# Kernel tuning notes

Hardware: AMD Instinct MI355X
Metric: run time of the kernel (lower is better)

Reference implementation:

```python
import jax, jax.numpy as jnp
from jax import lax
import numpy as np

EPS = 1e-5


def _fps(xyz, S):
    B, N, _ = xyz.shape

    def step(carry, _):
        dist, far = carry  # [B,N], [B]
        c = xyz[jnp.arange(B), far]               # [B,3]
        d = jnp.sum((xyz - c[:, None, :]) ** 2, -1)  # [B,N]
        dist = jnp.minimum(dist, d)
        nxt = jnp.argmax(dist, -1).astype(jnp.int32)
        return (dist, nxt), far

    init = (jnp.full((B, N), 1e10, xyz.dtype), jnp.zeros((B,), jnp.int32))
    _, idxs = lax.scan(step, init, None, length=S)
    return jnp.transpose(idxs)  # [B,S]


def _gather(pts, idx):
    # pts: [B,N,C], idx: [B,...] -> [B,...,C]
    return jax.vmap(lambda p, i: p[i])(pts, idx)


def _conv(x, W, b):
    # 1x1 Conv1d: x [M,Cin,L], W [Cout,Cin], b [Cout]
    return jnp.einsum('mcl,oc->mol', x, W) + b[None, :, None]


def _bn(x, g, b):
    # BatchNorm1d (training-mode batch stats, biased variance)
    mu = jnp.mean(x, (0, 2), keepdims=True)
    v = jnp.var(x, (0, 2), keepdims=True)
    return g[None, :, None] * (x - mu) / jnp.sqrt(v + EPS) + b[None, :, None]


def _forward(xyz, feature, affine_alpha, affine_beta, w_tr, b_tr, g_tr, be_tr,
             w1, b1, g1, be1, w2, b2, groups, k):
    xyz = jnp.transpose(xyz, (0, 2, 1))        # [B,N,3]
    feature = jnp.transpose(feature, (0, 2, 1))  # [B,N,D]
    B, N, _ = xyz.shape
    S = groups
    xyz_ng = lax.stop_gradient(xyz)  # cluster() runs under torch.no_grad
    fps_idx = _fps(xyz_ng, S)                        # [B,S]
    new_xyz = _gather(xyz_ng, fps_idx)               # [B,S,3] (detached)
    # squared-distance kNN: [B,S,N]
    sqr = (jnp.sum(new_xyz ** 2, -1)[:, :, None]
           + jnp.sum(xyz_ng ** 2, -1)[:, None, :]
           - 2.0 * jnp.einsum('bsc,bnc->bsn', new_xyz, xyz_ng))
    _, idx = lax.top_k(-sqr, k)                      # [B,S,k] smallest distances
    new_feature = _gather(feature, fps_idx)          # [B,S,D]
    grouped_xyz = _gather(xyz, idx)                  # [B,S,k,3]
    grouped_feature = _gather(feature, idx)          # [B,S,k,D]
    grouped_feature = jnp.concatenate([grouped_feature, grouped_xyz], -1)  # [B,S,k,D+3]
    # anchor normalization
    mean = jnp.concatenate([new_feature, new_xyz], -1)[:, :, None, :]  # [B,S,1,D+3]
    diff = grouped_feature - mean
    std = jnp.std(diff.reshape(B, -1), axis=-1, ddof=1)[:, None, None, None]
    gf = affine_alpha * (diff / (std + EPS)) + affine_beta
    # concat anchor feature -> [B,S,k,2D+3]
    D = new_feature.shape[-1]
    x = jnp.concatenate([gf, jnp.broadcast_to(new_feature[:, :, None, :], (B, S, k, D))], -1)
    d = x.shape[-1]
    # PreExtraction: [B,S,k,d] -> [B*S,d,k]
    x = jnp.transpose(x, (0, 1, 3, 2)).reshape(B * S, d, k)
    x = jax.nn.relu(_bn(_conv(x, w_tr, b_tr), g_tr, be_tr))
    y = jax.nn.relu(_bn(_conv(x, w1, b1), g1, be1))
    y = _conv(y, w2, b2)
    x = jax.nn.relu(y + x)
    x = jnp.max(x, -1).reshape(B, S, -1)             # adaptive_max_pool1d(1)
    return (jnp.transpose(new_xyz, (0, 2, 1)), jnp.transpose(x, (0, 2, 1)))


def setup_inputs() -> dict:
    key = jax.random.key(0)
    k0, k1, k2, k3, k4 = jax.random.split(key, 5)
    B, N, D = 8, 4096, 64
    return {
        'xyz': jax.random.normal(k0, (B, 3, N), jnp.float32),
        'feature': jax.random.normal(k1, (B, D, N), jnp.float32),
        'affine_alpha': jnp.ones((1, 1, 1, D + 3), jnp.float32),
        'affine_beta': jnp.zeros((1, 1, 1, D + 3), jnp.float32),
        'w_tr': 0.05 * jax.random.normal(k2, (D, 3 + 2 * D), jnp.float32),
        'b_tr': jnp.zeros((D,), jnp.float32),
        'g_tr': jnp.ones((D,), jnp.float32),
        'be_tr': jnp.zeros((D,), jnp.float32),
        'w1': 0.05 * jax.random.normal(k3, (D, D), jnp.float32),
        'b1': jnp.zeros((D,), jnp.float32),
        'g1': jnp.ones((D,), jnp.float32),
        'be1': jnp.zeros((D,), jnp.float32),
        'w2': 0.05 * jax.random.normal(k4, (D, D), jnp.float32),
        'b2': jnp.zeros((D,), jnp.float32),
        'groups': 1024,
        'k': 32,
    }


def reference(xyz, feature, affine_alpha, affine_beta, w_tr, b_tr, g_tr, be_tr,
              w1, b1, g1, be1, w2, b2, groups, k):
    return _forward(xyz, feature, affine_alpha, affine_beta, w_tr, b_tr, g_tr, be_tr,
                    w1, b1, g1, be1, w2, b2, groups, k)
```

## Files before the change

### kernel.cpp

```cpp
#include <hip/hip_runtime.h>
#include <cfloat>
#include <math.h>

#define B_ 8
#define N_ 4096
#define D_ 64
#define S_ 1024
#define K_ 32
#define CIN_ 131

template <int CTRL>
__device__ __forceinline__ unsigned long long dpp_u64(unsigned long long k) {
  int lo = (int)(unsigned int)k, hi = (int)(unsigned int)(k >> 32);
  lo = __builtin_amdgcn_update_dpp(lo, lo, CTRL, 0xf, 0xf, false);
  hi = __builtin_amdgcn_update_dpp(hi, hi, CTRL, 0xf, 0xf, false);
  return ((unsigned long long)(unsigned int)hi << 32) | (unsigned int)lo;
}

__device__ __forceinline__ float wave_max_f32_dpp(float v) {
  int x = __float_as_int(v);
#define STEP(ctrl)                                                        \
  {                                                                       \
    int t = __builtin_amdgcn_update_dpp(x, x, ctrl, 0xf, 0xf, false);     \
    v = fmaxf(v, __int_as_float(t));                                      \
    x = __float_as_int(v);                                                \
  }
  STEP(0x111)
  STEP(0x112)
  STEP(0x114)
  STEP(0x118)
  STEP(0x142)
  STEP(0x143)
#undef STEP
  return __int_as_float(__builtin_amdgcn_readlane(x, 63));
}

__global__ __launch_bounds__(256) void fps_kernel(const float* __restrict__ xyz,
                                                  int* __restrict__ fps_idx,
                                                  float* __restrict__ nxyz,
                                                  float* __restrict__ out0,
                                                  const float* __restrict__ feature,
                                                  float* __restrict__ featT) {
  const int tid = threadIdx.x;
  __shared__ __align__(16) float4 sp[N_];
  __shared__ int si[S_];
  __shared__ unsigned long long keyp[2][4];
  if (blockIdx.x >= 8) {
    const int blk = blockIdx.x - 8;
    const int b = blk >> 6, n0 = (blk & 63) * 64;
    float* tile = (float*)sp;
#pragma unroll
    for (int i = 0; i < 16; i++) {
      int c = i * 4 + (tid >> 6), nl = tid & 63;
      tile[c * 65 + nl] = feature[((size_t)b * 64 + c) * N_ + n0 + nl];
    }
    __syncthreads();
#pragma unroll
    for (int i = 0; i < 16; i++) {
      int nl = i * 4 + (tid >> 6), c = tid & 63;
      featT[((size_t)b * N_ + n0 + nl) * 64 + c] = tile[c * 65 + nl];
    }
    return;
  }
  const int b = blockIdx.x;
  const float* xb = xyz + (size_t)b * 3 * N_;
  const float4* xv = (const float4*)xb;
  float px[16], py[16], pz[16], dist[16];
#pragma unroll
  for (int q = 0; q < 4; q++) {
    float4 X = xv[4 * tid + q];
    float4 Y = xv[1024 + 4 * tid + q];
    float4 Z = xv[2048 + 4 * tid + q];
    px[4 * q + 0] = X.x; px[4 * q + 1] = X.y; px[4 * q + 2] = X.z; px[4 * q + 3] = X.w;
    py[4 * q + 0] = Y.x; py[4 * q + 1] = Y.y; py[4 * q + 2] = Y.z; py[4 * q + 3] = Y.w;
    pz[4 * q + 0] = Z.x; pz[4 * q + 1] = Z.y; pz[4 * q + 2] = Z.z; pz[4 * q + 3] = Z.w;
  }
#pragma unroll
  for (int i = 0; i < 16; i++) {
    dist[i] = 1e10f;
    sp[16 * tid + i] = make_float4(px[i], py[i], pz[i], 0.f);
  }
  if (tid == 0) si[0] = 0;
  __syncthreads();
  float cx = sp[0].x, cy = sp[0].y, cz = sp[0].z;
  const int wav = tid >> 6, lane = tid & 63;
  for (int s = 1; s < S_; s++) {
    float best = -1.0f;
    int bi = 16 * tid;
#pragma unroll
    for (int i = 0; i < 16; i++) {
      float dx = __fsub_rn(px[i], cx);
      float dy = __fsub_rn(py[i], cy);
      float dz = __fsub_rn(pz[i], cz);
      float d = __fadd_rn(__fadd_rn(__fmul_rn(dx, dx), __fmul_rn(dy, dy)), __fmul_rn(dz, dz));
      dist[i] = fminf(dist[i], d);
      if (dist[i] > best) { best = dist[i]; bi = 16 * tid + i; }
    }
    float wmax = wave_max_f32_dpp(best);
    unsigned long long m = __ballot(best == wmax);
    int l = __ffsll(m) - 1;
    int widx = __builtin_amdgcn_readlane(bi, l);
    if (lane == 0)
      keyp[s & 1][wav] =
          ((unsigned long long)(unsigned int)__float_as_int(wmax) << 32) |
          (unsigned int)(4095 - widx);
    __syncthreads();
    unsigned long long k = keyp[s & 1][lane & 3];
    unsigned long long t;
    t = dpp_u64<0xB1>(k); if (t > k) k = t;
    t = dpp_u64<0x4E>(k); if (t > k) k = t;
    int bix = 4095 - (int)(k & 0xfffull);
    if (tid == 0) si[s] = bix;
    float4 c = sp[bix];
    cx = c.x; cy = c.y; cz = c.z;
  }
  __syncthreads();
  for (int e = tid; e < S_; e += 256) {
    int n = si[e];
    fps_idx[b * S_ + e] = n;
    float4 c = sp[n];
    nxyz[(size_t)(b * S_ + e) * 3 + 0] = c.x;
    nxyz[(size_t)(b * S_ + e) * 3 + 1] = c.y;
    nxyz[(size_t)(b * S_ + e) * 3 + 2] = c.z;
    out0[(size_t)b * 3 * S_ + e] = c.x;
    out0[(size_t)b * 3 * S_ + S_ + e] = c.y;
    out0[(size_t)b * 3 * S_ + 2 * S_ + e] = c.z;
  }
}

__global__ __launch_bounds__(256) void knn_kernel(const float* __restrict__ xyz,
                                                  const float* __restrict__ nxyz,
                                                  int* __restrict__ knn,
                                                  const float* __restrict__ featT,
                                                  const int* __restrict__ fps_i,
                                                  float* __restrict__ nfeat) {
  const int bs = blockIdx.x, tid = threadIdx.x;
  if (bs >= 8192) {
    int e = (bs - 8192) * 256 + tid;
    int bsx = e >> 6, c = e & 63;
    int bq = bsx >> 10;
    int n = fps_i[bsx];
    nfeat[e] = featT[((size_t)bq * N_ + n) * 64 + c];
    return;
  }
  const int b = bs >> 10;
  const float* xb = xyz + (size_t)b * 3 * N_;
  const float cx = nxyz[(size_t)bs * 3], cy = nxyz[(size_t)bs * 3 + 1], cz = nxyz[(size_t)bs * 3 + 2];
  const float cn = __fadd_rn(__fadd_rn(__fmul_rn(cx, cx), __fmul_rn(cy, cy)), __fmul_rn(cz, cz));
  float d[16];
#pragma unroll
  for (int i = 0; i < 16; i++) {
    int n = i * 256 + tid;
    float px = xb[n], py = xb[N_ + n], pz = xb[2 * N_ + n];
    float pn = __fadd_rn(__fadd_rn(__fmul_rn(px, px), __fmul_rn(py, py)), __fmul_rn(pz, pz));
    float dot = __fadd_rn(__fadd_rn(__fmul_rn(cx, px), __fmul_rn(cy, py)), __fmul_rn(cz, pz));
    d[i] = __fsub_rn(__fadd_rn(cn, pn), __fmul_rn(2.0f, dot));
  }
  float mv = FLT_MAX;
  int mi = tid;
#pragma unroll
  for (int i = 0; i < 16; i++)
    if (d[i] < mv) { mv = d[i]; mi = i * 256 + tid; }
  __shared__ unsigned long long keyp[2][4];
  __shared__ int skk[K_];
  const int wav = tid >> 6, lane = tid & 63;
  for (int j = 0; j < K_; j++) {
    unsigned int u = __float_as_uint(mv);
    u ^= ((unsigned int)((int)u >> 31) | 0x80000000u);
    unsigned long long key = ((unsigned long long)u << 32) | (unsigned int)mi;
#pragma unroll
    for (int off = 32; off >= 1; off >>= 1) {
      unsigned long long ok = __shfl_xor(key, off);
      if (ok < key) key = ok;
    }
    if (lane == 0) keyp[j & 1][wav] = key;
    __syncthreads();
    unsigned long long kmin = keyp[j & 1][0];
#pragma unroll
    for (int w = 1; w < 4; w++) {
      unsigned long long k2 = keyp[j & 1][w];
      if (k2 < kmin) kmin = k2;
    }
    int g = (int)(kmin & 0xffffffffull);
    if (tid == 0) skk[j] = g;
    if ((g & 255) == tid) {
      int sl = g >> 8;
#pragma unroll
      for (int i = 0; i < 16; i++)
        if (i == sl) d[i] = FLT_MAX;
      mv = FLT_MAX; mi = tid;
#pragma unroll
      for (int i = 0; i < 16; i++)
        if (d[i] < mv) { mv = d[i]; mi = i * 256 + tid; }
    }
  }
  __syncthreads();
  if (tid < K_) knn[(size_t)bs * K_ + tid] = skk[tid];
}

__global__ __launch_bounds__(256) void gather_nf(const float* __restrict__ feature,
                                                 const int* __restrict__ fps_i,
                                                 float* __restrict__ nfeat) {
  int e = blockIdx.x * 256 + threadIdx.x;
  int b = e >> 16, rem = e & 65535;
  int s = rem >> 6, c = rem & 63;
  int n = fps_i[b * S_ + s];
  nfeat[e] = feature[((size_t)b * 64 + c) * N_ + n];
}

__global__ __launch_bounds__(256) void std_partial(const float* __restrict__ feature,
                                                   const float* __restrict__ xyz,
                                                   const float* __restrict__ nxyz,
                                                   const float* __restrict__ nfeat,
                                                   const int* __restrict__ knn,
                                                   float* __restrict__ outp) {
  const int blk = blockIdx.x, tid = threadIdx.x;
  const int b = blk >> 6, chunk = blk & 63;
  float s = 0.f, q = 0.f;
  for (int e = tid; e < 16 * K_ * 67; e += 256) {
    int so = e / (K_ * 67);
    int rem = e - so * (K_ * 67);
    int kk = rem / 67;
    int c = rem - kk * 67;
    int bs = b * S_ + chunk * 16 + so;
    int n = knn[(size_t)bs * K_ + kk];
    float raw = (c < 64) ? feature[((size_t)b * 64 + c) * N_ + n]
                         : xyz[((size_t)b * 3 + (c - 64)) * N_ + n];
    float anc = (c < 64) ? nfeat[(size_t)bs * 64 + c]
                         : nxyz[(size_t)bs * 3 + (c - 64)];
    float dd = raw - anc;
    s += dd; q += dd * dd;
  }
#pragma unroll
  for (int off = 32; off >= 1; off >>= 1) { s += __shfl_xor(s, off); q += __shfl_xor(q, off); }
  __shared__ float rs[4], rq[4];
  if ((tid & 63) == 0) { rs[tid >> 6] = s; rq[tid >> 6] = q; }
  __syncthreads();
  if (tid == 0) {
    outp[blk * 2] = rs[0] + rs[1] + rs[2] + rs[3];
    outp[blk * 2 + 1] = rq[0] + rq[1] + rq[2] + rq[3];
  }
}

__global__ void std_final(const float* __restrict__ part, float* __restrict__ invstd) {
  int b = threadIdx.x;
  if (b < B_) {
    double s = 0.0, q = 0.0;
    for (int i = 0; i < 64; i++) {
      s += (double)part[(b * 64 + i) * 2];
      q += (double)part[(b * 64 + i) * 2 + 1];
    }
    const double n = (double)(S_ * K_ * 67);
    double var = (q - s * s / n) / (n - 1.0);
    invstd[b] = (float)(1.0 / (sqrt(var) + 1e-5));
  }
}

template <int MODE>
__global__ __launch_bounds__(256, 2) void mlp_kernel(
    const float* __restrict__ feature, const float* __restrict__ xyz,
    const float* __restrict__ nxyz, const float* __restrict__ nfeat,
    const int* __restrict__ knn, const float* __restrict__ invstd,
    const float* __restrict__ alpha, const float* __restrict__ beta,
    const float* __restrict__ w_tr, const float* __restrict__ b_tr,
    const float* __restrict__ w1, const float* __restrict__ b1,
    const float* __restrict__ w2, const float* __restrict__ b2,
    const float* __restrict__ bn_tr, const float* __restrict__ bn_1,
    float* __restrict__ bnpart, float* __restrict__ out1) {
  __shared__ __align__(16) float pool[15556];
  float* Wt = pool;
  float* xin = pool + 8516;
  float* ub = xin;
  float* tb = pool + 8516 + 4192;
  float* part = pool + 8516 + 4192 + 2304;
  int* sknn = (int*)(part + 512);
  const int bs = blockIdx.x, tid = threadIdx.x;
  const int b = bs >> 10, s = bs & 1023;
  if (tid < K_) sknn[tid] = knn[(size_t)bs * K_ + tid];
  for (int e = tid; e < 64 * 131; e += 256) {
    int o = e / 131, c = e - o * 131;
    Wt[c * 65 + o] = w_tr[e];
  }
  __syncthreads();
  const float inv = invstd[b];
  for (int e = tid; e < CIN_ * K_; e += 256) {
    int c = e >> 5, kk = e & 31;
    float v;
    if (c < 67) {
      int n = sknn[kk];
      float raw = (c < 64) ? feature[((size_t)b * 64 + c) * N_ + n]
                           : xyz[((size_t)b * 3 + (c - 64)) * N_ + n];
      float anc = (c < 64) ? nfeat[(size_t)bs * 64 + c]
                           : nxyz[(size_t)bs * 3 + (c - 64)];
      v = alpha[c] * ((raw - anc) * inv) + beta[c];
    } else {
      v = nfeat[(size_t)bs * 64 + (c - 67)];
    }
    xin[e] = v;
  }
  __syncthreads();
  const int o = tid & 63, kkb = (tid >> 6) * 8;
  float acc[8];
  {
    float bv = b_tr[o];
#pragma unroll
    for (int j = 0; j < 8; j++) acc[j] = bv;
  }
  for (int c = 0; c < CIN_; c++) {
    float w = Wt[c * 65 + o];
    const float4 xa = *(const float4*)(xin + c * 32 + kkb);
    const float4 xb4 = *(const float4*)(xin + c * 32 + kkb + 4);
    acc[0] += w * xa.x; acc[1] += w * xa.y; acc[2] += w * xa.z; acc[3] += w * xa.w;
    acc[4] += w * xb4.x; acc[5] += w * xb4.y; acc[6] += w * xb4.z; acc[7] += w * xb4.w;
  }
  if (MODE == 0) {
    float s8 = 0.f, q8 = 0.f;
#pragma unroll
    for (int j = 0; j < 8; j++) { s8 += acc[j]; q8 += acc[j] * acc[j]; }
    part[(tid >> 6) * 64 + o] = s8;
    part[256 + (tid >> 6) * 64 + o] = q8;
    __syncthreads();
    if (tid < 64) {
      float ss = 0.f, qq = 0.f;
      for (int g = 0; g < 4; g++) { ss += part[g * 64 + tid]; qq += part[256 + g * 64 + tid]; }
      bnpart[(size_t)bs * 128 + tid] = ss;
      bnpart[(size_t)bs * 128 + 64 + tid] = qq;
    }
    return;
  }
  float tv[8];
  {
    float sc = bn_tr[o], sh = bn_tr[64 + o];
#pragma unroll
    for (int j = 0; j < 8; j++) {
      tv[j] = fmaxf(fmaf(sc, acc[j], sh), 0.f);
      tb[o * 36 + kkb + j] = tv[j];
    }
  }
  __syncthreads();
  for (int e = tid; e < 64 * 64; e += 256) {
    int oo = e >> 6, c = e & 63;
    Wt[c * 65 + oo] = w1[e];
  }
  __syncthreads();
  float acc2[8];
  {
    float bv = b1[o];
#pragma unroll
    for (int j = 0; j < 8; j++) acc2[j] = bv;
  }
  for (int c = 0; c < 64; c++) {
    float w = Wt[c * 65 + o];
    const float4 ta = *(const float4*)(tb + c * 36 + kkb);
    const float4 ta2 = *(const float4*)(tb + c * 36 + kkb + 4);
    acc2[0] += w * ta.x; acc2[1] += w * ta.y; acc2[2] += w * ta.z; acc2[3] += w * ta.w;
    acc2[4] += w * ta2.x; acc2[5] += w * ta2.y; acc2[6] += w * ta2.z; acc2[7] += w * ta2.w;
  }
  if (MODE == 1) {
    float s8 = 0.f, q8 = 0.f;
#pragma unroll
    for (int j = 0; j < 8; j++) { s8 += acc2[j]; q8 += acc2[j] * acc2[j]; }
    part[(tid >> 6) * 64 + o] = s8;
    part[256 + (tid >> 6) * 64 + o] = q8;
    __syncthreads();
    if (tid < 64) {
      float ss = 0.f, qq = 0.f;
      for (int g = 0; g < 4; g++) { ss += part[g * 64 + tid]; qq += part[256 + g * 64 + tid]; }
      bnpart[(size_t)bs * 128 + tid] = ss;
      bnpart[(size_t)bs * 128 + 64 + tid] = qq;
    }
    return;
  }
  {
    float sc = bn_1[o], sh = bn_1[64 + o];
#pragma unroll
    for (int j = 0; j < 8; j++) ub[o * 36 + kkb + j] = fmaxf(fmaf(sc, acc2[j], sh), 0.f);
  }
  __syncthreads();
  for (int e = tid; e < 64 * 64; e += 256) {
    int oo = e >> 6, c = e & 63;
    Wt[c * 65 + oo] = w2[e];
  }
  __syncthreads();
  float acc3[8];
  {
    float bv = b2[o];
#pragma unroll
    for (int j = 0; j < 8; j++) acc3[j] = bv;
  }
  for (int c = 0; c < 64; c++) {
    float w = Wt[c * 65 + o];
    const float4 ua = *(const float4*)(ub + c * 36 + kkb);
    const float4 ua2 = *(const float4*)(ub + c * 36 + kkb + 4);
    acc3[0] += w * ua.x; acc3[1] += w * ua.y; acc3[2] += w * ua.z; acc3[3] += w * ua.w;
    acc3[4] += w * ua2.x; acc3[5] += w * ua2.y; acc3[6] += w * ua2.z; acc3[7] += w * ua2.w;
  }
  float m = 0.f;
#pragma unroll
  for (int j = 0; j < 8; j++) m = fmaxf(m, fmaxf(acc3[j] + tv[j], 0.f));
  part[(tid >> 6) * 64 + o] = m;
  __syncthreads();
  if (tid < 64) {
    float mm = part[tid];
    for (int g = 1; g < 4; g++) mm = fmaxf(mm, part[g * 64 + tid]);
    out1[((size_t)b * 64 + tid) * S_ + s] = mm;
  }
}

__global__ __launch_bounds__(256) void bn_finalize(const float* __restrict__ part,
                                                   const float* __restrict__ g,
                                                   const float* __restrict__ be,
                                                   float* __restrict__ bnout) {
  const int ch = blockIdx.x, tid = threadIdx.x;
  double s = 0.0, q = 0.0;
  for (int i = tid; i < B_ * S_; i += 256) {
    s += (double)part[(size_t)i * 128 + ch];
    q += (double)part[(size_t)i * 128 + 64 + ch];
  }
#pragma unroll
  for (int off = 32; off >= 1; off >>= 1) { s += __shfl_xor(s, off); q += __shfl_xor(q, off); }
  __shared__ double ls[4], lq[4];
  if ((tid & 63) == 0) { ls[tid >> 6] = s; lq[tid >> 6] = q; }
  __syncthreads();
  if (tid == 0) {
    double Ssum = ls[0] + ls[1] + ls[2] + ls[3];
    double Qsum = lq[0] + lq[1] + lq[2] + lq[3];
    const double n = (double)(B_ * S_ * K_);
    double mu = Ssum / n;
    double var = Qsum / n - mu * mu;
    double sc = (double)g[ch] / sqrt(var + 1e-5);
    bnout[ch] = (float)sc;
    bnout[64 + ch] = (float)((double)be[ch] - mu * sc);
  }
}


__global__ __launch_bounds__(256) void prep_kernel(const float* __restrict__ featT,
                                                   const float* __restrict__ xyz,
                                                   const float* __restrict__ nxyz,
                                                   const float* __restrict__ nfeat,
                                                   const int* __restrict__ knn,
                                                   float* __restrict__ dcache,
                                                   float* __restrict__ outp) {
  const int blk = blockIdx.x, tid = threadIdx.x;
  __shared__ int sk[32];
  float s = 0.f, q = 0.f;
  const int c = tid & 63, qd = tid >> 6;
  for (int g = 0; g < 8; g++) {
    const int bs = blk * 8 + g, b = bs >> 10;
    if (tid < 32) sk[tid] = knn[(size_t)bs * K_ + tid];
    __syncthreads();
    float anc = nfeat[(size_t)bs * 64 + c];
#pragma unroll
    for (int it = 0; it < 8; it++) {
      int kk = it * 4 + qd;
      int n = sk[kk];
      float dd = featT[((size_t)b * N_ + n) * 64 + c] - anc;
      s += dd; q += dd * dd;
      dcache[((size_t)bs * 32 + kk) * 68 + c] = dd;
    }
    if (tid < 96) {
      int c3 = tid >> 5, kk = tid & 31;
      int n = sk[kk];
      float dd = xyz[((size_t)b * 3 + c3) * N_ + n] - nxyz[(size_t)bs * 3 + c3];
      s += dd; q += dd * dd;
      dcache[((size_t)bs * 32 + kk) * 68 + 64 + c3] = dd;
    }
    __syncthreads();
  }
#pragma unroll
  for (int off = 32; off >= 1; off >>= 1) { s += __shfl_xor(s, off); q += __shfl_xor(q, off); }
  __shared__ float rs[4], rq[4];
  if ((tid & 63) == 0) { rs[tid >> 6] = s; rq[tid >> 6] = q; }
  __syncthreads();
  if (tid == 0) {
    outp[blk * 2] = rs[0] + rs[1] + rs[2] + rs[3];
    outp[blk * 2 + 1] = rq[0] + rq[1] + rq[2] + rq[3];
  }
}

__global__ void std_final_c(const float* __restrict__ part, float* __restrict__ invstd) {
  int b = threadIdx.x;
  if (b < B_) {
    double s = 0.0, q = 0.0;
    for (int i = 0; i < 128; i++) {
      s += (double)part[(b * 128 + i) * 2];
      q += (double)part[(b * 128 + i) * 2 + 1];
    }
    const double n = (double)(S_ * K_ * 67);
    double var = (q - s * s / n) / (n - 1.0);
    invstd[b] = (float)(1.0 / (sqrt(var) + 1e-5));
  }
}

__global__ __launch_bounds__(256, 2) void mlp0c(
    const float* __restrict__ dcache, const float* __restrict__ nfeat,
    const float* __restrict__ invstd,
    const float* __restrict__ alpha, const float* __restrict__ beta,
    const float* __restrict__ w_tr, const float* __restrict__ b_tr,
    float* __restrict__ bnpart, float* __restrict__ tcache) {
  __shared__ __align__(16) float pool[13220];
  float* Wt = pool;
  float* xin = pool + 8516;
  float* part = pool + 8516 + 4192;
  const int bs = blockIdx.x, tid = threadIdx.x;
  const int b = bs >> 10;
  for (int e = tid; e < 64 * 131; e += 256) {
    int o = e / 131, c = e - o * 131;
    Wt[c * 65 + o] = w_tr[e];
  }
  const float inv = invstd[b];
  {
    const int c = tid & 63, qd = tid >> 6;
    float al = alpha[c], bev = beta[c];
#pragma unroll
    for (int it = 0; it < 8; it++) {
      int kk = it * 4 + qd;
      xin[c * 32 + kk] = al * (dcache[((size_t)bs * 32 + kk) * 68 + c] * inv) + bev;
    }
    if (tid < 96) {
      int c3 = 64 + (tid >> 5), kk = tid & 31;
      xin[c3 * 32 + kk] =
          alpha[c3] * (dcache[((size_t)bs * 32 + kk) * 68 + c3] * inv) + beta[c3];
    }
    for (int e = tid; e < 2048; e += 256) {
      int cc = 67 + (e >> 5), kk = e & 31;
      xin[cc * 32 + kk] = nfeat[(size_t)bs * 64 + (e >> 5)];
    }
  }
  __syncthreads();
  const int o = tid & 63, kkb = (tid >> 6) * 8;
  float acc[8];
  {
    float bv = b_tr[o];
#pragma unroll
    for (int j = 0; j < 8; j++) acc[j] = bv;
  }
  for (int c = 0; c < CIN_; c++) {
    float w = Wt[c * 65 + o];
    const float4 xa = *(const float4*)(xin + c * 32 + kkb);
    const float4 xb4 = *(const float4*)(xin + c * 32 + kkb + 4);
    acc[0] += w * xa.x; acc[1] += w * xa.y; acc[2] += w * xa.z; acc[3] += w * xa.w;
    acc[4] += w * xb4.x; acc[5] += w * xb4.y; acc[6] += w * xb4.z; acc[7] += w * xb4.w;
  }
  {
    float4* tp = (float4*)(tcache + ((size_t)bs * 64 + o) * 32 + kkb);
    tp[0] = make_float4(acc[0], acc[1], acc[2], acc[3]);
    tp[1] = make_float4(acc[4], acc[5], acc[6], acc[7]);
  }
  float s8 = 0.f, q8 = 0.f;
#pragma unroll
  for (int j = 0; j < 8; j++) { s8 += acc[j]; q8 += acc[j] * acc[j]; }
  part[(tid >> 6) * 64 + o] = s8;
  part[256 + (tid >> 6) * 64 + o] = q8;
  __syncthreads();
  if (tid < 64) {
    float ss = 0.f, qq = 0.f;
    for (int g = 0; g < 4; g++) { ss += part[g * 64 + tid]; qq += part[256 + g * 64 + tid]; }
    bnpart[(size_t)bs * 128 + tid] = ss;
    bnpart[(size_t)bs * 128 + 64 + tid] = qq;
  }
}

__global__ __launch_bounds__(256, 3) void mlp1c(
    const float* __restrict__ tcache, const float* __restrict__ bn_tr,
    const float* __restrict__ w1, const float* __restrict__ b1,
    float* __restrict__ bnpart, float* __restrict__ ucache) {
  __shared__ __align__(16) float pool[6976];
  float* Wt = pool;
  float* tb = pool + 4160;
  float* part = pool + 4160 + 2304;
  const int bs = blockIdx.x, tid = threadIdx.x;
  const int o = tid & 63, kkb = (tid >> 6) * 8;
  for (int e = tid; e < 64 * 64; e += 256) {
    int oo = e >> 6, c = e & 63;
    Wt[c * 65 + oo] = w1[e];
  }
  float t[8];
  {
    const float4* tp = (const float4*)(tcache + ((size_t)bs * 64 + o) * 32 + kkb);
    float4 a = tp[0], b4 = tp[1];
    t[0] = a.x; t[1] = a.y; t[2] = a.z; t[3] = a.w;
    t[4] = b4.x; t[5] = b4.y; t[6] = b4.z; t[7] = b4.w;
  }
  {
    float sc = bn_tr[o], sh = bn_tr[64 + o];
#pragma unroll
    for (int j = 0; j < 8; j++) tb[o * 36 + kkb + j] = fmaxf(fmaf(sc, t[j], sh), 0.f);
  }
  __syncthreads();
  float acc2[8];
  {
    float bv = b1[o];
#pragma unroll
    for (int j = 0; j < 8; j++) acc2[j] = bv;
  }
  for (int c = 0; c < 64; c++) {
    float w = Wt[c * 65 + o];
    const float4 ta = *(const float4*)(tb + c * 36 + kkb);
    const float4 ta2 = *(const float4*)(tb + c * 36 + kkb + 4);
    acc2[0] += w * ta.x; acc2[1] += w * ta.y; acc2[2] += w * ta.z; acc2[3] += w * ta.w;
    acc2[4] += w * ta2.x; acc2[5] += w * ta2.y; acc2[6] += w * ta2.z; acc2[7] += w * ta2.w;
  }
  {
    float4* up = (float4*)(ucache + ((size_t)bs * 64 + o) * 32 + kkb);
    up[0] = make_float4(acc2[0], acc2[1], acc2[2], acc2[3]);
    up[1] = make_float4(acc2[4], acc2[5], acc2[6], acc2[7]);
  }
  float s8 = 0.f, q8 = 0.f;
#pragma unroll
  for (int j = 0; j < 8; j++) { s8 += acc2[j]; q8 += acc2[j] * acc2[j]; }
  part[(tid >> 6) * 64 + o] = s8;
  part[256 + (tid >> 6) * 64 + o] = q8;
  __syncthreads();
  if (tid < 64) {
    float ss = 0.f, qq = 0.f;
    for (int g = 0; g < 4; g++) { ss += part[g * 64 + tid]; qq += part[256 + g * 64 + tid]; }
    bnpart[(size_t)bs * 128 + tid] = ss;
    bnpart[(size_t)bs * 128 + 64 + tid] = qq;
  }
}

__global__ __launch_bounds__(256, 3) void mlp2c(
    const float* __restrict__ tcache, const float* __restrict__ ucache,
    const float* __restrict__ bn_tr, const float* __restrict__ bn_1,
    const float* __restrict__ w2, const float* __restrict__ b2,
    float* __restrict__ out1) {
  __shared__ __align__(16) float pool[6976];
  float* Wt = pool;
  float* ub = pool + 4160;
  float* part = pool + 4160 + 2304;
  const int bs = blockIdx.x, tid = threadIdx.x;
  const int b = bs >> 10, s = bs & 1023;
  const int o = tid & 63, kkb = (tid >> 6) * 8;
  for (int e = tid; e < 64 * 64; e += 256) {
    int oo = e >> 6, c = e & 63;
    Wt[c * 65 + oo] = w2[e];
  }
  {
    const float4* up = (const float4*)(ucache + ((size_t)bs * 64 + o) * 32 + kkb);
    float4 a = up[0], b4 = up[1];
    float u[8] = {a.x, a.y, a.z, a.w, b4.x, b4.y, b4.z, b4.w};
    float sc = bn_1[o], sh = bn_1[64 + o];
#pragma unroll
    for (int j = 0; j < 8; j++) ub[o * 36 + kkb + j] = fmaxf(fmaf(sc, u[j], sh), 0.f);
  }
  __syncthreads();
  float acc3[8];
  {
    float bv = b2[o];
#pragma unroll
    for (int j = 0; j < 8; j++) acc3[j] = bv;
  }
  for (int c = 0; c < 64; c++) {
    float w = Wt[c * 65 + o];
    const float4 ua = *(const float4*)(ub + c * 36 + kkb);
    const float4 ua2 = *(const float4*)(ub + c * 36 + kkb + 4);
    acc3[0] += w * ua.x; acc3[1] += w * ua.y; acc3[2] += w * ua.z; acc3[3] += w * ua.w;
    acc3[4] += w * ua2.x; acc3[5] += w * ua2.y; acc3[6] += w * ua2.z; acc3[7] += w * ua2.w;
  }
  float tv[8];
  {
    const float4* tp = (const float4*)(tcache + ((size_t)bs * 64 + o) * 32 + kkb);
    float4 a = tp[0], b4 = tp[1];
    float t[8] = {a.x, a.y, a.z, a.w, b4.x, b4.y, b4.z, b4.w};
    float sc = bn_tr[o], sh = bn_tr[64 + o];
#pragma unroll
    for (int j = 0; j < 8; j++) tv[j] = fmaxf(fmaf(sc, t[j], sh), 0.f);
  }
  float m = 0.f;
#pragma unroll
  for (int j = 0; j < 8; j++) m = fmaxf(m, fmaxf(acc3[j] + tv[j], 0.f));
  part[(tid >> 6) * 64 + o] = m;
  __syncthreads();
  if (tid < 64) {
    float mm = part[tid];
    for (int g = 1; g < 4; g++) mm = fmaxf(mm, part[g * 64 + tid]);
    out1[((size_t)b * 64 + tid) * S_ + s] = mm;
  }
}

extern "C" void kernel_launch(void* const* d_in, const int* in_sizes, int n_in,
                              void* d_out, int out_size, void* d_ws, size_t ws_size,
                              hipStream_t stream) {
  const float* xyz = (const float*)d_in[0];
  const float* feature = (const float*)d_in[1];
  const float* alpha = (const float*)d_in[2];
  const float* beta = (const float*)d_in[3];
  const float* w_tr = (const float*)d_in[4];
  const float* b_tr = (const float*)d_in[5];
  const float* g_tr = (const float*)d_in[6];
  const float* be_tr = (const float*)d_in[7];
  const float* w1 = (const float*)d_in[8];
  const float* b1 = (const float*)d_in[9];
  const float* g1 = (const float*)d_in[10];
  const float* be1 = (const float*)d_in[11];
  const float* w2 = (const float*)d_in[12];
  const float* b2 = (const float*)d_in[13];

  char* ws = (char*)d_ws;
  int* fps_i = (int*)(ws);
  float* nxyz = (float*)(ws + 32768);
  float* nfeat = (float*)(ws + 131072);
  int* knn = (int*)(ws + 2228224);
  float* stdpart = (float*)(ws + 3276800);
  float* invstd = (float*)(ws + 3280896);
  float* bn_tr = (float*)(ws + 3280960);
  float* bn_1 = (float*)(ws + 3281472);
  float* bnpart = (float*)(ws + 3281984);
  float* featT = (float*)(ws + 7476288);
  float* dcache = (float*)(ws + 15864896);
  float* tcache = (float*)(ws + 87168064);
  float* ucache = (float*)(ws + 154276928);
  float* stdpart_c = (float*)(ws + 221385792);

  float* out0 = (float*)d_out;
  float* out1 = out0 + B_ * 3 * S_;

  const bool big = (ws_size >= 221393984ull);

  if (big) {
    fps_kernel<<<8 + 512, 256, 0, stream>>>(xyz, fps_i, nxyz, out0, feature, featT);
    knn_kernel<<<8192 + 2048, 256, 0, stream>>>(xyz, nxyz, knn, featT, fps_i, nfeat);
    prep_kernel<<<1024, 256, 0, stream>>>(featT, xyz, nxyz, nfeat, knn, dcache, stdpart_c);
    std_final_c<<<1, 64, 0, stream>>>(stdpart_c, invstd);
    mlp0c<<<B_ * S_, 256, 0, stream>>>(dcache, nfeat, invstd, alpha, beta, w_tr, b_tr,
                                       bnpart, tcache);
    bn_finalize<<<64, 256, 0, stream>>>(bnpart, g_tr, be_tr, bn_tr);
    mlp1c<<<B_ * S_, 256, 0, stream>>>(tcache, bn_tr, w1, b1, bnpart, ucache);
    bn_finalize<<<64, 256, 0, stream>>>(bnpart, g1, be1, bn_1);
    mlp2c<<<B_ * S_, 256, 0, stream>>>(tcache, ucache, bn_tr, bn_1, w2, b2, out1);
  } else {
    fps_kernel<<<8, 256, 0, stream>>>(xyz, fps_i, nxyz, out0, feature, featT);
    gather_nf<<<(B_ * S_ * D_) / 256, 256, 0, stream>>>(feature, fps_i, nfeat);
    knn_kernel<<<8192, 256, 0, stream>>>(xyz, nxyz, knn, nullptr, nullptr, nullptr);
    std_partial<<<B_ * 64, 256, 0, stream>>>(feature, xyz, nxyz, nfeat, knn, stdpart);
    std_final<<<1, 64, 0, stream>>>(stdpart, invstd);
    mlp_kernel<0><<<B_ * S_, 256, 0, stream>>>(feature, xyz, nxyz, nfeat, knn, invstd,
                                               alpha, beta, w_tr, b_tr, w1, b1, w2, b2,
                                               bn_tr, bn_1, bnpart, out1);
    bn_finalize<<<64, 256, 0, stream>>>(bnpart, g_tr, be_tr, bn_tr);
    mlp_kernel<1><<<B_ * S_, 256, 0, stream>>>(feature, xyz, nxyz, nfeat, knn, invstd,
                                               alpha, beta, w_tr, b_tr, w1, b1, w2, b2,
                                               bn_tr, bn_1, bnpart, out1);
    bn_finalize<<<64, 256, 0, stream>>>(bnpart, g1, be1, bn_1);
    mlp_kernel<2><<<B_ * S_, 256, 0, stream>>>(feature, xyz, nxyz, nfeat, knn, invstd,
                                               alpha, beta, w_tr, b_tr, w1, b1, w2, b2,
                                               bn_tr, bn_1, bnpart, out1);
  }
}
```

Baseline: 1.167 ms.

## Fuse FPS, kNN, gather and prep into one persistent kernel with flag-based dataflow

Merges the FPS, feature transpose, kNN, anchor gather and prep/statistics kernels into a single launch. FPS blocks publish their results in chunks of 64 centroids through release flags, and the downstream blocks spin on acquire counters, so kNN and gather can start before FPS finishes. The aim is to hide the long serial FPS latency behind the kNN work and drop the launch gaps. It depends on the FPS blocks being scheduled before the waiting blocks, and the spinning blocks occupy CU slots while they wait.

```diff
diff --git a/kernel.cpp b/kernel.cpp
--- a/kernel.cpp
+++ b/kernel.cpp
@@ -35,33 +35,253 @@
   return __int_as_float(__builtin_amdgcn_readlane(x, 63));
 }
 
+__device__ __forceinline__ void wait_count(const unsigned int* p, unsigned int val) {
+  while (__hip_atomic_load(p, __ATOMIC_ACQUIRE, __HIP_MEMORY_SCOPE_AGENT) < val)
+    __builtin_amdgcn_s_sleep(8);
+}
+__device__ __forceinline__ void rel_add(unsigned int* p) {
+  __hip_atomic_fetch_add(p, 1u, __ATOMIC_RELEASE, __HIP_MEMORY_SCOPE_AGENT);
+}
+
+__global__ __launch_bounds__(256) void stage1_kernel(
+    const float* __restrict__ xyz, const float* __restrict__ feature,
+    int* __restrict__ fps_idx, float* __restrict__ nxyz, float* __restrict__ out0,
+    float* __restrict__ featT, int* __restrict__ knn, float* __restrict__ nfeat,
+    float* __restrict__ dcache, float* __restrict__ outp,
+    unsigned int* __restrict__ flags, unsigned int* __restrict__ kcount,
+    unsigned int* __restrict__ gcount, unsigned int* __restrict__ tcount) {
+  const int bid = blockIdx.x, tid = threadIdx.x;
+  __shared__ __align__(16) float4 sp[N_];
+  __shared__ int si64[64];
+  __shared__ unsigned long long kbuf[2][4];
+
+  if (bid < 8) {
+    const int b = bid;
+    const float* xb = xyz + (size_t)b * 3 * N_;
+    const float4* xv = (const float4*)xb;
+    float px[16], py[16], pz[16], dist[16];
+#pragma unroll
+    for (int q = 0; q < 4; q++) {
+      float4 X = xv[4 * tid + q];
+      float4 Y = xv[1024 + 4 * tid + q];
+      float4 Z = xv[2048 + 4 * tid + q];
+      px[4 * q + 0] = X.x; px[4 * q + 1] = X.y; px[4 * q + 2] = X.z; px[4 * q + 3] = X.w;
+      py[4 * q + 0] = Y.x; py[4 * q + 1] = Y.y; py[4 * q + 2] = Y.z; py[4 * q + 3] = Y.w;
+      pz[4 * q + 0] = Z.x; pz[4 * q + 1] = Z.y; pz[4 * q + 2] = Z.z; pz[4 * q + 3] = Z.w;
+    }
+#pragma unroll
+    for (int i = 0; i < 16; i++) {
+      dist[i] = 1e10f;
+      sp[16 * tid + i] = make_float4(px[i], py[i], pz[i], 0.f);
+    }
+    if (tid == 0) si64[0] = 0;
+    __syncthreads();
+    float cx = sp[0].x, cy = sp[0].y, cz = sp[0].z;
+    const int wav = tid >> 6, lane = tid & 63;
+    for (int s = 1; s < S_; s++) {
+      float best = -1.0f;
+      int bi = 16 * tid;
+#pragma unroll
+      for (int i = 0; i < 16; i++) {
+        float dx = __fsub_rn(px[i], cx);
+        float dy = __fsub_rn(py[i], cy);
+        float dz = __fsub_rn(pz[i], cz);
+        float d = __fadd_rn(__fadd_rn(__fmul_rn(dx, dx), __fmul_rn(dy, dy)), __fmul_rn(dz, dz));
+        dist[i] = fminf(dist[i], d);
+        if (dist[i] > best) { best = dist[i]; bi = 16 * tid + i; }
+      }
+      float wmax = wave_max_f32_dpp(best);
+      unsigned long long m = __ballot(best == wmax);
+      int l = __ffsll(m) - 1;
+      int widx = __builtin_amdgcn_readlane(bi, l);
+      if (lane == 0)
+        kbuf[s & 1][wav] =
+            ((unsigned long long)(unsigned int)__float_as_int(wmax) << 32) |
+            (unsigned int)(4095 - widx);
+      __syncthreads();
+      unsigned long long k = kbuf[s & 1][lane & 3];
+      unsigned long long t;
+      t = dpp_u64<0xB1>(k); if (t > k) k = t;
+      t = dpp_u64<0x4E>(k); if (t > k) k = t;
+      int bix = 4095 - (int)(k & 0xfffull);
+      if (tid == 0) si64[s & 63] = bix;
+      float4 c = sp[bix];
+      cx = c.x; cy = c.y; cz = c.z;
+      if ((s & 63) == 63) {
+        __syncthreads();
+        if (tid < 64) {
+          int ss = (s - 63) + tid;
+          int gs = b * S_ + ss;
+          int n = si64[tid];
+          float4 cc = sp[n];
+          fps_idx[gs] = n;
+          nxyz[(size_t)gs * 3 + 0] = cc.x;
+          nxyz[(size_t)gs * 3 + 1] = cc.y;
+          nxyz[(size_t)gs * 3 + 2] = cc.z;
+          out0[(size_t)b * 3 * S_ + ss] = cc.x;
+          out0[(size_t)b * 3 * S_ + S_ + ss] = cc.y;
+          out0[(size_t)b * 3 * S_ + 2 * S_ + ss] = cc.z;
+        }
+        __syncthreads();
+        if (tid == 0) {
+          __threadfence();
+          __hip_atomic_store(&flags[b * 16 + (s >> 6)], 1u, __ATOMIC_RELEASE,
+                             __HIP_MEMORY_SCOPE_AGENT);
+        }
+      }
+    }
+    return;
+  }
+  if (bid < 520) {
+    const int blk = bid - 8;
+    const int b = blk >> 6, n0 = (blk & 63) * 64;
+    float* tile = (float*)sp;
+#pragma unroll
+    for (int i = 0; i < 16; i++) {
+      int c = i * 4 + (tid >> 6), nl = tid & 63;
+      tile[c * 65 + nl] = feature[((size_t)b * 64 + c) * N_ + n0 + nl];
+    }
+    __syncthreads();
+#pragma unroll
+    for (int i = 0; i < 16; i++) {
+      int nl = i * 4 + (tid >> 6), c = tid & 63;
+      featT[((size_t)b * N_ + n0 + nl) * 64 + c] = tile[c * 65 + nl];
+    }
+    __syncthreads();
+    if (tid == 0) rel_add(tcount);
+    return;
+  }
+  if (bid < 8712) {
+    const int bs = bid - 520;
+    if (tid == 0) wait_count(&flags[bs >> 6], 1);
+    __syncthreads();
+    const int b = bs >> 10;
+    const float* xb = xyz + (size_t)b * 3 * N_;
+    const float cx = nxyz[(size_t)bs * 3], cy = nxyz[(size_t)bs * 3 + 1],
+                cz = nxyz[(size_t)bs * 3 + 2];
+    const float cn = __fadd_rn(__fadd_rn(__fmul_rn(cx, cx), __fmul_rn(cy, cy)), __fmul_rn(cz, cz));
+    float d[16];
+#pragma unroll
+    for (int i = 0; i < 16; i++) {
+      int n = i * 256 + tid;
+      float px = xb[n], py = xb[N_ + n], pz = xb[2 * N_ + n];
+      float pn = __fadd_rn(__fadd_rn(__fmul_rn(px, px), __fmul_rn(py, py)), __fmul_rn(pz, pz));
+      float dot = __fadd_rn(__fadd_rn(__fmul_rn(cx, px), __fmul_rn(cy, py)), __fmul_rn(cz, pz));
+      d[i] = __fsub_rn(__fadd_rn(cn, pn), __fmul_rn(2.0f, dot));
+    }
+    float mv = FLT_MAX;
+    int mi = tid;
+#pragma unroll
+    for (int i = 0; i < 16; i++)
+      if (d[i] < mv) { mv = d[i]; mi = i * 256 + tid; }
+    int* skk = si64;
+    const int wav = tid >> 6, lane = tid & 63;
+    for (int j = 0; j < K_; j++) {
+      unsigned int u = __float_as_uint(mv);
+      u ^= ((unsigned int)((int)u >> 31) | 0x80000000u);
+      unsigned long long key = ((unsigned long long)u << 32) | (unsigned int)mi;
+#pragma unroll
+      for (int off = 32; off >= 1; off >>= 1) {
+        unsigned long long ok = __shfl_xor(key, off);
+        if (ok < key) key = ok;
+      }
+      if (lane == 0) kbuf[j & 1][wav] = key;
+      __syncthreads();
+      unsigned long long kmin = kbuf[j & 1][0];
+#pragma unroll
+      for (int w = 1; w < 4; w++) {
+        unsigned long long k2 = kbuf[j & 1][w];
+        if (k2 < kmin) kmin = k2;
+      }
+      int g = (int)(kmin & 0xffffffffull);
+      if (tid == 0) skk[j] = g;
+      if ((g & 255) == tid) {
+        int sl = g >> 8;
+#pragma unroll
+        for (int i = 0; i < 16; i++)
+          if (i == sl) d[i] = FLT_MAX;
+        mv = FLT_MAX; mi = tid;
+#pragma unroll
+        for (int i = 0; i < 16; i++)
+          if (d[i] < mv) { mv = d[i]; mi = i * 256 + tid; }
+      }
+    }
+    __syncthreads();
+    if (tid < K_) knn[(size_t)bs * K_ + tid] = skk[tid];
+    __syncthreads();
+    if (tid == 0) rel_add(&kcount[bs >> 6]);
+    return;
+  }
+  if (bid < 10760) {
+    const int j = bid - 8712;
+    if (tid == 0) {
+      wait_count(tcount, 512);
+      wait_count(&flags[j >> 4], 1);
+    }
+    __syncthreads();
+    int e = j * 256 + tid;
+    int bsx = e >> 6, c = e & 63;
+    int bq = bsx >> 10;
+    int n = fps_idx[bsx];
+    nfeat[e] = featT[((size_t)bq * N_ + n) * 64 + c];
+    __syncthreads();
+    if (tid == 0) rel_add(&gcount[j >> 4]);
+    return;
+  }
+  {
+    const int blk = bid - 10760;
+    if (tid == 0) {
+      wait_count(tcount, 512);
+      wait_count(&kcount[blk >> 3], 64);
+      wait_count(&gcount[blk >> 3], 16);
+    }
+    __syncthreads();
+    int* sk = si64;
+    float s = 0.f, q = 0.f;
+    const int c = tid & 63, qd = tid >> 6;
+    for (int g = 0; g < 8; g++) {
+      const int bs = blk * 8 + g, b = bs >> 10;
+      if (tid < 32) sk[tid] = knn[(size_t)bs * K_ + tid];
+      __syncthreads();
+      float anc = nfeat[(size_t)bs * 64 + c];
+#pragma unroll
+      for (int it = 0; it < 8; it++) {
+        int kk = it * 4 + qd;
+        int n = sk[kk];
+        float dd = featT[((size_t)b * N_ + n) * 64 + c] - anc;
+        s += dd; q += dd * dd;
+        dcache[((size_t)bs * 32 + kk) * 68 + c] = dd;
+      }
+      if (tid < 96) {
+        int c3 = tid >> 5, kk = tid & 31;
+        int n = sk[kk];
+        float dd = xyz[((size_t)b * 3 + c3) * N_ + n] - nxyz[(size_t)bs * 3 + c3];
+        s += dd; q += dd * dd;
+        dcache[((size_t)bs * 32 + kk) * 68 + 64 + c3] = dd;
+      }
+      __syncthreads();
+    }
+#pragma unroll
+    for (int off = 32; off >= 1; off >>= 1) { s += __shfl_xor(s, off); q += __shfl_xor(q, off); }
+    float* rs = (float*)kbuf;
+    float* rq = rs + 4;
+    if ((tid & 63) == 0) { rs[tid >> 6] = s; rq[tid >> 6] = q; }
+    __syncthreads();
+    if (tid == 0) {
+      outp[blk * 2] = rs[0] + rs[1] + rs[2] + rs[3];
+      outp[blk * 2 + 1] = rq[0] + rq[1] + rq[2] + rq[3];
+    }
+  }
+}
+
 __global__ __launch_bounds__(256) void fps_kernel(const float* __restrict__ xyz,
                                                   int* __restrict__ fps_idx,
                                                   float* __restrict__ nxyz,
-                                                  float* __restrict__ out0,
-                                                  const float* __restrict__ feature,
-                                                  float* __restrict__ featT) {
+                                                  float* __restrict__ out0) {
   const int tid = threadIdx.x;
   __shared__ __align__(16) float4 sp[N_];
   __shared__ int si[S_];
   __shared__ unsigned long long keyp[2][4];
-  if (blockIdx.x >= 8) {
-    const int blk = blockIdx.x - 8;
-    const int b = blk >> 6, n0 = (blk & 63) * 64;
-    float* tile = (float*)sp;
-#pragma unroll
-    for (int i = 0; i < 16; i++) {
-      int c = i * 4 + (tid >> 6), nl = tid & 63;
-      tile[c * 65 + nl] = feature[((size_t)b * 64 + c) * N_ + n0 + nl];
-    }
-    __syncthreads();
-#pragma unroll
-    for (int i = 0; i < 16; i++) {
-      int nl = i * 4 + (tid >> 6), c = tid & 63;
-      featT[((size_t)b * N_ + n0 + nl) * 64 + c] = tile[c * 65 + nl];
-    }
-    return;
-  }
   const int b = blockIdx.x;
   const float* xb = xyz + (size_t)b * 3 * N_;
   const float4* xv = (const float4*)xb;
@@ -130,19 +350,8 @@
 
 __global__ __launch_bounds__(256) void knn_kernel(const float* __restrict__ xyz,
                                                   const float* __restrict__ nxyz,
-                                                  int* __restrict__ knn,
-                                                  const float* __restrict__ featT,
-                                                  const int* __restrict__ fps_i,
-                                                  float* __restrict__ nfeat) {
+                                                  int* __restrict__ knn) {
   const int bs = blockIdx.x, tid = threadIdx.x;
-  if (bs >= 8192) {
-    int e = (bs - 8192) * 256 + tid;
-    int bsx = e >> 6, c = e & 63;
-    int bq = bsx >> 10;
-    int n = fps_i[bsx];
-    nfeat[e] = featT[((size_t)bq * N_ + n) * 64 + c];
-    return;
-  }
   const int b = bs >> 10;
   const float* xb = xyz + (size_t)b * 3 * N_;
   const float cx = nxyz[(size_t)bs * 3], cy = nxyz[(size_t)bs * 3 + 1], cz = nxyz[(size_t)bs * 3 + 2];
@@ -434,51 +643,6 @@
   }
 }
 
-
-__global__ __launch_bounds__(256) void prep_kernel(const float* __restrict__ featT,
-                                                   const float* __restrict__ xyz,
-                                                   const float* __restrict__ nxyz,
-                                                   const float* __restrict__ nfeat,
-                                                   const int* __restrict__ knn,
-                                                   float* __restrict__ dcache,
-                                                   float* __restrict__ outp) {
-  const int blk = blockIdx.x, tid = threadIdx.x;
-  __shared__ int sk[32];
-  float s = 0.f, q = 0.f;
-  const int c = tid & 63, qd = tid >> 6;
-  for (int g = 0; g < 8; g++) {
-    const int bs = blk * 8 + g, b = bs >> 10;
-    if (tid < 32) sk[tid] = knn[(size_t)bs * K_ + tid];
-    __syncthreads();
-    float anc = nfeat[(size_t)bs * 64 + c];
-#pragma unroll
-    for (int it = 0; it < 8; it++) {
-      int kk = it * 4 + qd;
-      int n = sk[kk];
-      float dd = featT[((size_t)b * N_ + n) * 64 + c] - anc;
-      s += dd; q += dd * dd;
-      dcache[((size_t)bs * 32 + kk) * 68 + c] = dd;
-    }
-    if (tid < 96) {
-      int c3 = tid >> 5, kk = tid & 31;
-      int n = sk[kk];
-      float dd = xyz[((size_t)b * 3 + c3) * N_ + n] - nxyz[(size_t)bs * 3 + c3];
-      s += dd; q += dd * dd;
-      dcache[((size_t)bs * 32 + kk) * 68 + 64 + c3] = dd;
-    }
-    __syncthreads();
-  }
-#pragma unroll
-  for (int off = 32; off >= 1; off >>= 1) { s += __shfl_xor(s, off); q += __shfl_xor(q, off); }
-  __shared__ float rs[4], rq[4];
-  if ((tid & 63) == 0) { rs[tid >> 6] = s; rq[tid >> 6] = q; }
-  __syncthreads();
-  if (tid == 0) {
-    outp[blk * 2] = rs[0] + rs[1] + rs[2] + rs[3];
-    outp[blk * 2 + 1] = rq[0] + rq[1] + rq[2] + rq[3];
-  }
-}
-
 __global__ void std_final_c(const float* __restrict__ part, float* __restrict__ invstd) {
   int b = threadIdx.x;
   if (b < B_) {
@@ -713,16 +877,21 @@
   float* tcache = (float*)(ws + 87168064);
   float* ucache = (float*)(ws + 154276928);
   float* stdpart_c = (float*)(ws + 221385792);
+  unsigned int* flags = (unsigned int*)(ws + 221393984);
+  unsigned int* kcount = (unsigned int*)(ws + 221394496);
+  unsigned int* gcount = (unsigned int*)(ws + 221395008);
+  unsigned int* tcount = (unsigned int*)(ws + 221395520);
 
   float* out0 = (float*)d_out;
   float* out1 = out0 + B_ * 3 * S_;
 
-  const bool big = (ws_size >= 221393984ull);
+  const bool big = (ws_size >= 221395584ull);
 
   if (big) {
-    fps_kernel<<<8 + 512, 256, 0, stream>>>(xyz, fps_i, nxyz, out0, feature, featT);
-    knn_kernel<<<8192 + 2048, 256, 0, stream>>>(xyz, nxyz, knn, featT, fps_i, nfeat);
-    prep_kernel<<<1024, 256, 0, stream>>>(featT, xyz, nxyz, nfeat, knn, dcache, stdpart_c);
+    hipMemsetAsync(ws + 221393984, 0, 1600, stream);
+    stage1_kernel<<<8 + 512 + 8192 + 2048 + 1024, 256, 0, stream>>>(
+        xyz, feature, fps_i, nxyz, out0, featT, knn, nfeat, dcache, stdpart_c,
+        flags, kcount, gcount, tcount);
     std_final_c<<<1, 64, 0, stream>>>(stdpart_c, invstd);
     mlp0c<<<B_ * S_, 256, 0, stream>>>(dcache, nfeat, invstd, alpha, beta, w_tr, b_tr,
                                        bnpart, tcache);
@@ -731,9 +900,9 @@
     bn_finalize<<<64, 256, 0, stream>>>(bnpart, g1, be1, bn_1);
     mlp2c<<<B_ * S_, 256, 0, stream>>>(tcache, ucache, bn_tr, bn_1, w2, b2, out1);
   } else {
-    fps_kernel<<<8, 256, 0, stream>>>(xyz, fps_i, nxyz, out0, feature, featT);
+    fps_kernel<<<8, 256, 0, stream>>>(xyz, fps_i, nxyz, out0);
     gather_nf<<<(B_ * S_ * D_) / 256, 256, 0, stream>>>(feature, fps_i, nfeat);
-    knn_kernel<<<8192, 256, 0, stream>>>(xyz, nxyz, knn, nullptr, nullptr, nullptr);
+    knn_kernel<<<8192, 256, 0, stream>>>(xyz, nxyz, knn);
     std_partial<<<B_ * 64, 256, 0, stream>>>(feature, xyz, nxyz, nfeat, knn, stdpart);
     std_final<<<1, 64, 0, stream>>>(stdpart, invstd);
     mlp_kernel<0><<<B_ * S_, 256, 0, stream>>>(feature, xyz, nxyz, nfeat, knn, invstd,
```

New measurement: 1.402 ms. 20.2% more time.

## Bucket FPS points into spatial cells and skip cells via bounding-box bounds

Applied to the files above, without the earlier changes.

The FPS kernel now sorts points into a 4x4x4 grid of 64 cells of 64 points each, held in shared memory with per-point running distances. For each new centroid it computes a lower bound on the distance to each cell's bounding box and skips cells that cannot change their cached maximum. Only the remaining cells are recomputed, with a packed 64-bit key (distance, original index, position) reduced through DPP. This is meant to cut the per-iteration distance work of the serial 1023-step loop. In exchange it adds per-iteration shared-memory traffic, a data-dependent loop that may diverge across waves, and a 0.999 slack factor on the bound that carries tie and precision risk.

```diff
diff --git a/kernel.cpp b/kernel.cpp
--- a/kernel.cpp
+++ b/kernel.cpp
@@ -17,22 +17,15 @@
   return ((unsigned long long)(unsigned int)hi << 32) | (unsigned int)lo;
 }
 
-__device__ __forceinline__ float wave_max_f32_dpp(float v) {
-  int x = __float_as_int(v);
-#define STEP(ctrl)                                                        \
-  {                                                                       \
-    int t = __builtin_amdgcn_update_dpp(x, x, ctrl, 0xf, 0xf, false);     \
-    v = fmaxf(v, __int_as_float(t));                                      \
-    x = __float_as_int(v);                                                \
-  }
-  STEP(0x111)
-  STEP(0x112)
-  STEP(0x114)
-  STEP(0x118)
-  STEP(0x142)
-  STEP(0x143)
-#undef STEP
-  return __int_as_float(__builtin_amdgcn_readlane(x, 63));
+__device__ __forceinline__ unsigned long long wave_max_u64_dpp(unsigned long long k) {
+  unsigned long long t;
+  t = dpp_u64<0x111>(k); if (t > k) k = t;
+  t = dpp_u64<0x112>(k); if (t > k) k = t;
+  t = dpp_u64<0x114>(k); if (t > k) k = t;
+  t = dpp_u64<0x118>(k); if (t > k) k = t;
+  t = dpp_u64<0x142>(k); if (t > k) k = t;
+  t = dpp_u64<0x143>(k); if (t > k) k = t;
+  return k;
 }
 
 __global__ __launch_bounds__(256) void fps_kernel(const float* __restrict__ xyz,
@@ -43,8 +36,13 @@
                                                   float* __restrict__ featT) {
   const int tid = threadIdx.x;
   __shared__ __align__(16) float4 sp[N_];
+  __shared__ unsigned short sidx[N_];
+  __shared__ unsigned short spos[S_];
   __shared__ int si[S_];
-  __shared__ unsigned long long keyp[2][4];
+  __shared__ float bbx0[64], bbx1[64], bby0[64], bby1[64], bbz0[64], bbz1[64];
+  __shared__ unsigned long long gkey[2][64];
+  __shared__ int hist[64];
+  __shared__ float red[24];
   if (blockIdx.x >= 8) {
     const int blk = blockIdx.x - 8;
     const int b = blk >> 6, n0 = (blk & 63) * 64;
@@ -63,9 +61,10 @@
     return;
   }
   const int b = blockIdx.x;
+  const int lane = tid & 63, wav = tid >> 6;
   const float* xb = xyz + (size_t)b * 3 * N_;
   const float4* xv = (const float4*)xb;
-  float px[16], py[16], pz[16], dist[16];
+  float px[16], py[16], pz[16];
 #pragma unroll
   for (int q = 0; q < 4; q++) {
     float4 X = xv[4 * tid + q];
@@ -75,50 +74,125 @@
     py[4 * q + 0] = Y.x; py[4 * q + 1] = Y.y; py[4 * q + 2] = Y.z; py[4 * q + 3] = Y.w;
     pz[4 * q + 0] = Z.x; pz[4 * q + 1] = Z.y; pz[4 * q + 2] = Z.z; pz[4 * q + 3] = Z.w;
   }
+  float mnx = px[0], mxx = px[0], mny = py[0], mxy = py[0], mnz = pz[0], mxz = pz[0];
+#pragma unroll
+  for (int i = 1; i < 16; i++) {
+    mnx = fminf(mnx, px[i]); mxx = fmaxf(mxx, px[i]);
+    mny = fminf(mny, py[i]); mxy = fmaxf(mxy, py[i]);
+    mnz = fminf(mnz, pz[i]); mxz = fmaxf(mxz, pz[i]);
+  }
+#pragma unroll
+  for (int off = 32; off >= 1; off >>= 1) {
+    mnx = fminf(mnx, __shfl_xor(mnx, off)); mxx = fmaxf(mxx, __shfl_xor(mxx, off));
+    mny = fminf(mny, __shfl_xor(mny, off)); mxy = fmaxf(mxy, __shfl_xor(mxy, off));
+    mnz = fminf(mnz, __shfl_xor(mnz, off)); mxz = fmaxf(mxz, __shfl_xor(mxz, off));
+  }
+  if (lane == 0) {
+    red[wav * 6 + 0] = mnx; red[wav * 6 + 1] = mxx;
+    red[wav * 6 + 2] = mny; red[wav * 6 + 3] = mxy;
+    red[wav * 6 + 4] = mnz; red[wav * 6 + 5] = mxz;
+  }
+  if (tid < 64) hist[tid] = 0;
+  __syncthreads();
+  const float Bx0 = fminf(fminf(red[0], red[6]), fminf(red[12], red[18]));
+  const float Bx1 = fmaxf(fmaxf(red[1], red[7]), fmaxf(red[13], red[19]));
+  const float By0 = fminf(fminf(red[2], red[8]), fminf(red[14], red[20]));
+  const float By1 = fmaxf(fmaxf(red[3], red[9]), fmaxf(red[15], red[21]));
+  const float Bz0 = fminf(fminf(red[4], red[10]), fminf(red[16], red[22]));
+  const float Bz1 = fmaxf(fmaxf(red[5], red[11]), fmaxf(red[17], red[23]));
+  const float sxs = 4.0f / fmaxf(Bx1 - Bx0, 1e-20f);
+  const float sys = 4.0f / fmaxf(By1 - By0, 1e-20f);
+  const float szs = 4.0f / fmaxf(Bz1 - Bz0, 1e-20f);
+  int cid[16];
 #pragma unroll
   for (int i = 0; i < 16; i++) {
-    dist[i] = 1e10f;
-    sp[16 * tid + i] = make_float4(px[i], py[i], pz[i], 0.f);
-  }
-  if (tid == 0) si[0] = 0;
-  __syncthreads();
-  float cx = sp[0].x, cy = sp[0].y, cz = sp[0].z;
-  const int wav = tid >> 6, lane = tid & 63;
+    int ix = min(3, (int)((px[i] - Bx0) * sxs));
+    int iy = min(3, (int)((py[i] - By0) * sys));
+    int iz = min(3, (int)((pz[i] - Bz0) * szs));
+    cid[i] = (ix << 4) | (iy << 2) | iz;
+    atomicAdd(&hist[cid[i]], 1);
+  }
+  __syncthreads();
+  if (tid == 0) {
+    int acc = 0;
+    for (int g = 0; g < 64; g++) { int h = hist[g]; hist[g] = acc; acc += h; }
+  }
+  __syncthreads();
+#pragma unroll
+  for (int i = 0; i < 16; i++) {
+    int pos = atomicAdd(&hist[cid[i]], 1);
+    sp[pos] = make_float4(px[i], py[i], pz[i], 1e10f);
+    int orig = 16 * tid + i;
+    sidx[pos] = (unsigned short)orig;
+    if (orig == 0) { spos[0] = (unsigned short)pos; si[0] = 0; }
+  }
+  __syncthreads();
+  if (tid < 64) {
+    float4 P = sp[tid * 64];
+    float a0 = P.x, a1 = P.x, b0 = P.y, b1 = P.y, c0 = P.z, c1 = P.z;
+    for (int j = 1; j < 64; j++) {
+      P = sp[tid * 64 + j];
+      a0 = fminf(a0, P.x); a1 = fmaxf(a1, P.x);
+      b0 = fminf(b0, P.y); b1 = fmaxf(b1, P.y);
+      c0 = fminf(c0, P.z); c1 = fmaxf(c1, P.z);
+    }
+    bbx0[tid] = a0; bbx1[tid] = a1;
+    bby0[tid] = b0; bby1[tid] = b1;
+    bbz0[tid] = c0; bbz1[tid] = c1;
+  }
+  __syncthreads();
+  const float gx0 = bbx0[lane], gx1 = bbx1[lane];
+  const float gy0 = bby0[lane], gy1 = bby1[lane];
+  const float gz0 = bbz0[lane], gz1 = bbz1[lane];
+  unsigned long long gq = ((unsigned long long)__float_as_uint(1e10f)) << 24;
+  float4 c0v = sp[spos[0]];
+  float cx = c0v.x, cy = c0v.y, cz = c0v.z;
+  const unsigned long long stripe = 0x1111111111111111ULL << wav;
   for (int s = 1; s < S_; s++) {
-    float best = -1.0f;
-    int bi = 16 * tid;
-#pragma unroll
-    for (int i = 0; i < 16; i++) {
-      float dx = __fsub_rn(px[i], cx);
-      float dy = __fsub_rn(py[i], cy);
-      float dz = __fsub_rn(pz[i], cz);
+    const int p = s & 1;
+    float tx = fmaxf(fmaxf(__fsub_rn(gx0, cx), __fsub_rn(cx, gx1)), 0.f);
+    float ty = fmaxf(fmaxf(__fsub_rn(gy0, cy), __fsub_rn(cy, gy1)), 0.f);
+    float tz = fmaxf(fmaxf(__fsub_rn(gz0, cz), __fsub_rn(cz, gz1)), 0.f);
+    float lb = tx * tx + ty * ty + tz * tz;
+    float gmax = __uint_as_float((unsigned int)(gq >> 24));
+    bool upd = (lb * 0.999f) < gmax;
+    unsigned long long mask = __ballot(upd);
+    if (wav == 0 && !upd) gkey[p][lane] = gq;
+    unsigned long long m = mask & stripe;
+    while (m) {
+      int g = __ffsll(m) - 1; m &= m - 1;
+      int pp = g * 64 + lane;
+      float4 P = sp[pp];
+      unsigned int oi = sidx[pp];
+      float dx = __fsub_rn(P.x, cx), dy = __fsub_rn(P.y, cy), dz = __fsub_rn(P.z, cz);
       float d = __fadd_rn(__fadd_rn(__fmul_rn(dx, dx), __fmul_rn(dy, dy)), __fmul_rn(dz, dz));
-      dist[i] = fminf(dist[i], d);
-      if (dist[i] > best) { best = dist[i]; bi = 16 * tid + i; }
-    }
-    float wmax = wave_max_f32_dpp(best);
-    unsigned long long m = __ballot(best == wmax);
-    int l = __ffsll(m) - 1;
-    int widx = __builtin_amdgcn_readlane(bi, l);
-    if (lane == 0)
-      keyp[s & 1][wav] =
-          ((unsigned long long)(unsigned int)__float_as_int(wmax) << 32) |
-          (unsigned int)(4095 - widx);
+      float nd = fminf(P.w, d);
+      sp[pp].w = nd;
+      unsigned long long k = ((unsigned long long)__float_as_uint(nd) << 24) |
+                             ((unsigned long long)(4095u - oi) << 12) | (unsigned int)pp;
+      k = wave_max_u64_dpp(k);
+      if (lane == 63) gkey[p][g] = k;
+    }
     __syncthreads();
-    unsigned long long k = keyp[s & 1][lane & 3];
-    unsigned long long t;
-    t = dpp_u64<0xB1>(k); if (t > k) k = t;
-    t = dpp_u64<0x4E>(k); if (t > k) k = t;
-    int bix = 4095 - (int)(k & 0xfffull);
-    if (tid == 0) si[s] = bix;
-    float4 c = sp[bix];
-    cx = c.x; cy = c.y; cz = c.z;
+    unsigned long long kq = gkey[p][lane];
+    gq = kq;
+    unsigned long long kk = wave_max_u64_dpp(kq);
+    unsigned int lo = (unsigned int)__builtin_amdgcn_readlane((int)(unsigned int)kk, 63);
+    unsigned int hi = (unsigned int)__builtin_amdgcn_readlane((int)(unsigned int)(kk >> 32), 63);
+    unsigned long long kwin = ((unsigned long long)hi << 32) | lo;
+    int pos = (int)(kwin & 0xfffull);
+    if (tid == 0) {
+      si[s] = 4095 - (int)((kwin >> 12) & 0xfffull);
+      spos[s] = (unsigned short)pos;
+    }
+    float4 C = sp[pos];
+    cx = C.x; cy = C.y; cz = C.z;
   }
   __syncthreads();
   for (int e = tid; e < S_; e += 256) {
     int n = si[e];
+    float4 c = sp[spos[e]];
     fps_idx[b * S_ + e] = n;
-    float4 c = sp[n];
     nxyz[(size_t)(b * S_ + e) * 3 + 0] = c.x;
     nxyz[(size_t)(b * S_ + e) * 3 + 1] = c.y;
     nxyz[(size_t)(b * S_ + e) * 3 + 2] = c.z;
@@ -433,7 +507,6 @@
     bnout[64 + ch] = (float)((double)be[ch] - mu * sc);
   }
 }
-
 
 __global__ __launch_bounds__(256) void prep_kernel(const float* __restrict__ featT,
                                                    const float* __restrict__ xyz,
```

Result: slower. 2.236 ms (+91.7%).
